# Kernel tuning notes

Measured on AMD Instinct MI355X. Metric: run time of the kernel, lower is better.

The kernel has to match this reference:

```python
import jax, jax.numpy as jnp
import numpy as np

B, S, D = 2, 2048, 1024
H = 16
HD = D // H


def setup_inputs() -> dict:
    key = jax.random.key(0)
    k1, k2, k3 = jax.random.split(key, 3)
    x = jax.random.normal(k1, (B, S, D), dtype=jnp.float32)
    # nn.Linear(d, 3d, bias=False): weight [3d, d]; y = x @ W.T
    w_qkv = jax.random.normal(k2, (3 * D, D), dtype=jnp.float32) * (D ** -0.5)
    w_out = jax.random.normal(k3, (D, D), dtype=jnp.float32) * (D ** -0.5)
    return {"x": x, "w_qkv": w_qkv, "w_out": w_out}


def reference(x, w_qkv, w_out):
    batch, seq_len, _ = x.shape
    qkv = jnp.einsum('bsd,ed->bse', x, w_qkv)  # [B,S,3D]
    q, k, v = jnp.split(qkv, 3, axis=-1)
    # [B,S,D] -> [B,H,S,HD]
    def heads(t):
        return t.reshape(batch, seq_len, H, HD).transpose(0, 2, 1, 3)
    q, k, v = heads(q), heads(k), heads(v)
    scale = HD ** -0.5
    attn = jnp.einsum('bhqd,bhkd->bhqk', q, k) * scale  # [B,H,S,S]
    causal = jnp.triu(jnp.ones((seq_len, seq_len), dtype=bool), k=1)
    attn = jnp.where(causal, -jnp.inf, attn)
    attn = jax.nn.softmax(attn, axis=-1)
    out = jnp.einsum('bhqk,bhkd->bhqd', attn, v)  # [B,H,S,HD]
    out = out.transpose(0, 2, 1, 3).reshape(batch, seq_len, D)
    return jnp.einsum('bsd,ed->bse', out, w_out)
```

## Files before the change

### kernel.cpp

```cpp
#include <hip/hip_runtime.h>

#define NUM_B 2
#define SEQ   2048
#define DIM   1024
#define NH    16
#define HD    64

typedef __attribute__((ext_vector_type(8))) short short8;
typedef __attribute__((ext_vector_type(4))) float floatx4;
typedef unsigned short us;

#define SOFTMAX_SHIFT 12.0f

__device__ __forceinline__ us f2bf(float f) {
    unsigned u = __float_as_uint(f);
    u += 0x7fffu + ((u >> 16) & 1u);
    return (us)(u >> 16);
}
__device__ __forceinline__ us f2bf_t(float f) {
    return (us)(__float_as_uint(f) >> 16);
}

#define GLD16(gptr, lptr) __builtin_amdgcn_global_load_lds( \
    (__attribute__((address_space(1))) unsigned int*)(gptr), \
    (__attribute__((address_space(3))) unsigned int*)(lptr), 16, 0, 0)

__global__ __launch_bounds__(256) void cast_all(
    const float* __restrict__ x, const float* __restrict__ wq,
    const float* __restrict__ wo, us* __restrict__ xb,
    us* __restrict__ wqb, us* __restrict__ wob)
{
    int i = blockIdx.x * 256 + threadIdx.x;
    const float* src; us* dst; int off;
    if (i < 524288)      { src = x;  dst = xb;  off = i; }
    else if (i < 917504) { src = wq; dst = wqb; off = i - 524288; }
    else                 { src = wo; dst = wob; off = i - 917504; }
    const float4* p = (const float4*)src + (size_t)off * 2;
    float4 f0 = p[0];
    float4 f1 = p[1];
    short8 v;
    v[0] = (short)f2bf(f0.x); v[1] = (short)f2bf(f0.y);
    v[2] = (short)f2bf(f0.z); v[3] = (short)f2bf(f0.w);
    v[4] = (short)f2bf(f1.x); v[5] = (short)f2bf(f1.y);
    v[6] = (short)f2bf(f1.z); v[7] = (short)f2bf(f1.w);
    *(short8*)(dst + (size_t)off * 8) = v;
}

__global__ __launch_bounds__(256, 2) void gemm_qkv(
    const us* __restrict__ A, const us* __restrict__ Bw,
    us* __restrict__ qb, us* __restrict__ kb, us* __restrict__ vt)
{
    __shared__ us As[128 * 64];
    __shared__ us Bs[128 * 64];
    const int t = threadIdx.x;
    const int lane = t & 63, w = t >> 6;
    const int l16 = lane & 15, quad = lane >> 4;
    const int wr = (w >> 1) * 64, wc = (w & 1) * 64;
    const int m0 = blockIdx.y * 128, n0 = blockIdx.x * 128;
    const bool isV = (blockIdx.x >= 16);
    const int srow = lane >> 3;
    const int soff = ((lane & 7) ^ srow) << 3;
    const int rsw  = l16 & 7;

    floatx4 acc[4][4];
    #pragma unroll
    for (int i = 0; i < 4; ++i)
        #pragma unroll
        for (int j = 0; j < 4; ++j) acc[i][j] = (floatx4){0.f, 0.f, 0.f, 0.f};

    for (int k0 = 0; k0 < DIM; k0 += 64) {
        #pragma unroll
        for (int c = 0; c < 4; ++c) {
            int chunk = w * 4 + c;
            int row = chunk * 8 + srow;
            GLD16(A  + (size_t)(m0 + row) * DIM + k0 + soff, &As[chunk * 512]);
            GLD16(Bw + (size_t)(n0 + row) * DIM + k0 + soff, &Bs[chunk * 512]);
        }
        __syncthreads();
        #pragma unroll
        for (int s = 0; s < 2; ++s) {
            short8 af[4], bf[4];
            #pragma unroll
            for (int i = 0; i < 4; ++i)
                af[i] = *(const short8*)&As[(wr + i * 16 + l16) * 64 + (((s * 4 + quad) ^ rsw) << 3)];
            #pragma unroll
            for (int j = 0; j < 4; ++j)
                bf[j] = *(const short8*)&Bs[(wc + j * 16 + l16) * 64 + (((s * 4 + quad) ^ rsw) << 3)];
            if (!isV) {
                #pragma unroll
                for (int i = 0; i < 4; ++i)
                    #pragma unroll
                    for (int j = 0; j < 4; ++j)
                        acc[i][j] = __builtin_amdgcn_mfma_f32_16x16x32_bf16(af[i], bf[j], acc[i][j], 0, 0, 0);
            } else {
                #pragma unroll
                for (int i = 0; i < 4; ++i)
                    #pragma unroll
                    for (int j = 0; j < 4; ++j)
                        acc[i][j] = __builtin_amdgcn_mfma_f32_16x16x32_bf16(bf[j], af[i], acc[i][j], 0, 0, 0);
            }
        }
        __syncthreads();
    }

    if (!isV) {
        const int which = n0 >> 10;
        const float sc = (which == 0) ? 0.125f : 1.0f;
        us* dst = (which == 0) ? qb : kb;
        #pragma unroll
        for (int i = 0; i < 4; ++i) {
            #pragma unroll
            for (int j = 0; j < 4; ++j) {
                int e = n0 + wc + j * 16 + l16;
                int h  = (e >> 6) & 15;
                int hd = e & 63;
                #pragma unroll
                for (int r = 0; r < 4; ++r) {
                    int m = m0 + wr + i * 16 + quad * 4 + r;
                    int b = m >> 11, s = m & 2047;
                    dst[((size_t)((b * NH + h) * SEQ + s) << 6) + hd] = f2bf(acc[i][j][r] * sc);
                }
            }
        }
    } else {
        #pragma unroll
        for (int i = 0; i < 4; ++i) {
            int m = m0 + wr + i * 16 + l16;
            int b = m >> 11, s = m & 2047;
            #pragma unroll
            for (int j = 0; j < 4; ++j) {
                int e0 = (n0 - 2048) + wc + j * 16 + quad * 4;
                #pragma unroll
                for (int r = 0; r < 4; ++r) {
                    int e = e0 + r;
                    int h = e >> 6, hd = e & 63;
                    vt[((size_t)((b * NH + h) * HD + hd) << 11) + s] = f2bf(acc[i][j][r]);
                }
            }
        }
    }
}

__global__ __launch_bounds__(256, 2) void gemm_out(
    const us* __restrict__ A, const us* __restrict__ Bw, float* __restrict__ outp)
{
    __shared__ us As[64 * 64];
    __shared__ us Bs[128 * 64];
    const int t = threadIdx.x;
    const int lane = t & 63, w = t >> 6;
    const int l16 = lane & 15, quad = lane >> 4;
    const int wr = (w >> 1) * 32, wc = (w & 1) * 64;
    const int m0 = blockIdx.y * 64, n0 = blockIdx.x * 128;
    const int srow = lane >> 3;
    const int soff = ((lane & 7) ^ srow) << 3;
    const int rsw  = l16 & 7;

    floatx4 acc[2][4];
    #pragma unroll
    for (int i = 0; i < 2; ++i)
        #pragma unroll
        for (int j = 0; j < 4; ++j) acc[i][j] = (floatx4){0.f, 0.f, 0.f, 0.f};

    for (int k0 = 0; k0 < DIM; k0 += 64) {
        #pragma unroll
        for (int c = 0; c < 2; ++c) {
            int chunk = w * 2 + c;
            int row = chunk * 8 + srow;
            GLD16(A + (size_t)(m0 + row) * DIM + k0 + soff, &As[chunk * 512]);
        }
        #pragma unroll
        for (int c = 0; c < 4; ++c) {
            int chunk = w * 4 + c;
            int row = chunk * 8 + srow;
            GLD16(Bw + (size_t)(n0 + row) * DIM + k0 + soff, &Bs[chunk * 512]);
        }
        __syncthreads();
        #pragma unroll
        for (int s = 0; s < 2; ++s) {
            short8 af[2], bf[4];
            #pragma unroll
            for (int i = 0; i < 2; ++i)
                af[i] = *(const short8*)&As[(wr + i * 16 + l16) * 64 + (((s * 4 + quad) ^ rsw) << 3)];
            #pragma unroll
            for (int j = 0; j < 4; ++j)
                bf[j] = *(const short8*)&Bs[(wc + j * 16 + l16) * 64 + (((s * 4 + quad) ^ rsw) << 3)];
            #pragma unroll
            for (int i = 0; i < 2; ++i)
                #pragma unroll
                for (int j = 0; j < 4; ++j)
                    acc[i][j] = __builtin_amdgcn_mfma_f32_16x16x32_bf16(af[i], bf[j], acc[i][j], 0, 0, 0);
        }
        __syncthreads();
    }

    #pragma unroll
    for (int i = 0; i < 2; ++i)
        #pragma unroll
        for (int j = 0; j < 4; ++j) {
            int n = n0 + wc + j * 16 + l16;
            #pragma unroll
            for (int r = 0; r < 4; ++r) {
                int m = m0 + wr + i * 16 + quad * 4 + r;
                outp[(size_t)m * DIM + n] = acc[i][j][r];
            }
        }
}

__global__ __launch_bounds__(256, 4) void attn(
    const us* __restrict__ qb, const us* __restrict__ kb,
    const us* __restrict__ vt, us* __restrict__ ob)
{
    __shared__ us Ks[2][64 * 64];
    __shared__ us Vs[2][64 * 64];
    __shared__ us Ps[4 * 16 * 72];
    const int t = threadIdx.x;
    const int lane = t & 63, w = t >> 6;
    const int l16 = lane & 15, quad = lane >> 4;
    const int idx = blockIdx.x;
    const int qt = 31 - (idx >> 5);
    const int bh = idx & 31;
    const int b = bh >> 4, h = bh & 15;
    const int q0 = qt << 6;
    const int r0 = q0 + w * 16;
    const int rowb = r0 + quad * 4;
    const size_t base = (size_t)bh * SEQ * HD;
    const us* qbh = qb + base;
    const us* kbh = kb + base;
    const us* vth = vt + base;
    us* Pp = Ps + w * 16 * 72;
    const int srow = lane >> 3;
    const int soff = ((lane & 7) ^ srow) << 3;
    const int rsw  = l16 & 7;

    short8 qa[2];
    #pragma unroll
    for (int s = 0; s < 2; ++s)
        qa[s] = *(const short8*)(qbh + (size_t)(r0 + l16) * HD + s * 32 + quad * 8);

    floatx4 o[4];
    #pragma unroll
    for (int j = 0; j < 4; ++j) o[j] = (floatx4){0.f, 0.f, 0.f, 0.f};
    float lrow[4] = {0.f, 0.f, 0.f, 0.f};

    #pragma unroll
    for (int c = 0; c < 2; ++c) {
        int chunk = w * 2 + c;
        int row = chunk * 8 + srow;
        GLD16(kbh + (size_t)row * HD + soff, &Ks[0][chunk * 512]);
        GLD16(vth + (size_t)row * SEQ + soff, &Vs[0][chunk * 512]);
    }
    __syncthreads();

    for (int kt = 0; kt <= qt; ++kt) {
        const int cur = kt & 1;
        if (kt < qt) {
            const int j0n = (kt + 1) << 6;
            #pragma unroll
            for (int c = 0; c < 2; ++c) {
                int chunk = w * 2 + c;
                int row = chunk * 8 + srow;
                GLD16(kbh + (size_t)(j0n + row) * HD + soff, &Ks[cur ^ 1][chunk * 512]);
                GLD16(vth + (size_t)row * SEQ + j0n + soff, &Vs[cur ^ 1][chunk * 512]);
            }
        }

        floatx4 sf[4];
        #pragma unroll
        for (int j = 0; j < 4; ++j)
            sf[j] = (floatx4){-SOFTMAX_SHIFT, -SOFTMAX_SHIFT, -SOFTMAX_SHIFT, -SOFTMAX_SHIFT};
        #pragma unroll
        for (int s = 0; s < 2; ++s)
            #pragma unroll
            for (int j = 0; j < 4; ++j) {
                short8 kf = *(const short8*)&Ks[cur][(j * 16 + l16) * 64 + (((s * 4 + quad) ^ rsw) << 3)];
                sf[j] = __builtin_amdgcn_mfma_f32_16x16x32_bf16(qa[s], kf, sf[j], 0, 0, 0);
            }

        float p[4][4];
        #pragma unroll
        for (int j = 0; j < 4; ++j)
            #pragma unroll
            for (int r = 0; r < 4; ++r) p[j][r] = sf[j][r];

        if (kt == qt) {
            const int j0 = kt << 6;
            #pragma unroll
            for (int j = 0; j < 4; ++j) {
                int colg = j0 + j * 16 + l16;
                #pragma unroll
                for (int r = 0; r < 4; ++r)
                    if (colg > rowb + r) p[j][r] = -1e30f;
            }
        }

        #pragma unroll
        for (int j = 0; j < 4; ++j)
            #pragma unroll
            for (int r = 0; r < 4; ++r) {
                p[j][r] = __expf(p[j][r]);
                Pp[(quad * 4 + r) * 72 + j * 16 + l16] = f2bf_t(p[j][r]);
            }
        #pragma unroll
        for (int r = 0; r < 4; ++r)
            lrow[r] += (p[0][r] + p[1][r]) + (p[2][r] + p[3][r]);

        #pragma unroll
        for (int s = 0; s < 2; ++s) {
            short8 pf = *(const short8*)&Pp[l16 * 72 + s * 32 + quad * 8];
            #pragma unroll
            for (int j = 0; j < 4; ++j) {
                short8 vf = *(const short8*)&Vs[cur][(j * 16 + l16) * 64 + (((s * 4 + quad) ^ rsw) << 3)];
                o[j] = __builtin_amdgcn_mfma_f32_16x16x32_bf16(pf, vf, o[j], 0, 0, 0);
            }
        }
        __syncthreads();
    }

    #pragma unroll
    for (int r = 0; r < 4; ++r) {
        float l = lrow[r];
        l += __shfl_xor(l, 1);
        l += __shfl_xor(l, 2);
        l += __shfl_xor(l, 4);
        l += __shfl_xor(l, 8);
        float inv = 1.0f / l;
        #pragma unroll
        for (int j = 0; j < 4; ++j) {
            float val = o[j][r] * inv;
            ob[(size_t)(b * SEQ + rowb + r) * DIM + h * HD + j * 16 + l16] = f2bf(val);
        }
    }
}

extern "C" void kernel_launch(void* const* d_in, const int* in_sizes, int n_in,
                              void* d_out, int out_size, void* d_ws, size_t ws_size,
                              hipStream_t stream) {
    const float* x     = (const float*)d_in[0];
    const float* w_qkv = (const float*)d_in[1];
    const float* w_out = (const float*)d_in[2];
    float* out = (float*)d_out;
    us* ws = (us*)d_ws;

    const size_t M1 = (size_t)1024 * 1024;
    us* xb  = ws;
    us* wqb = xb  + 4 * M1;
    us* wob = wqb + 3 * M1;
    us* qb  = wob + 1 * M1;
    us* kb  = qb  + 4 * M1;
    us* vt  = kb  + 4 * M1;
    us* obf = vt  + 4 * M1;

    cast_all<<<4096, 256, 0, stream>>>(x, w_qkv, w_out, xb, wqb, wob);
    gemm_qkv<<<dim3(24, 32), 256, 0, stream>>>(xb, wqb, qb, kb, vt);
    attn<<<1024, 256, 0, stream>>>(qb, kb, vt, obf);
    gemm_out<<<dim3(8, 64), 256, 0, stream>>>(obf, wob, out);
}
```

Baseline: 170.0 us.

## Rewrite QKV GEMM as 256x256 double-buffered 8-wave pipeline; add MFMA priority hints

The QKV projection GEMM moves from 128x128 tiles with 4 waves and a single LDS buffer to 256x256 tiles with 8 waves and double-buffered LDS. Each K-step is split into four quadrant phases, with global-to-LDS loads of the next tile interleaved and fenced by explicit vmcnt waits and barriers. s_setprio is raised around MFMA blocks in both the GEMM and the attention kernel. The goal is to hide load latency and raise per-block operand reuse, at the cost of only 192 blocks on the GPU, 128 KB of LDS per block, and heavy accumulator register pressure.

After: 189.7 us. 1.12x slower.

```diff
diff --git a/kernel.cpp b/kernel.cpp
--- a/kernel.cpp
+++ b/kernel.cpp
@@ -24,6 +24,10 @@
 #define GLD16(gptr, lptr) __builtin_amdgcn_global_load_lds( \
     (__attribute__((address_space(1))) unsigned int*)(gptr), \
     (__attribute__((address_space(3))) unsigned int*)(lptr), 16, 0, 0)
+
+#define VMW(n) asm volatile("s_waitcnt vmcnt(" #n ")" ::: "memory")
+#define BAR()  __builtin_amdgcn_s_barrier()
+#define SETP(p) __builtin_amdgcn_s_setprio(p)
 
 __global__ __launch_bounds__(256) void cast_all(
     const float* __restrict__ x, const float* __restrict__ wq,
@@ -46,61 +50,104 @@
     *(short8*)(dst + (size_t)off * 8) = v;
 }
 
-__global__ __launch_bounds__(256, 2) void gemm_qkv(
+__global__ __launch_bounds__(512, 2) void gemm_qkv(
     const us* __restrict__ A, const us* __restrict__ Bw,
     us* __restrict__ qb, us* __restrict__ kb, us* __restrict__ vt)
 {
-    __shared__ us As[128 * 64];
-    __shared__ us Bs[128 * 64];
+    __shared__ us As[2][256 * 64];
+    __shared__ us Bs[2][256 * 64];
     const int t = threadIdx.x;
     const int lane = t & 63, w = t >> 6;
     const int l16 = lane & 15, quad = lane >> 4;
-    const int wr = (w >> 1) * 64, wc = (w & 1) * 64;
-    const int m0 = blockIdx.y * 128, n0 = blockIdx.x * 128;
-    const bool isV = (blockIdx.x >= 16);
+    const int wr = (w >> 2) * 128, wc = (w & 3) * 64;
+    const int m0 = blockIdx.y * 256, n0 = blockIdx.x * 256;
+    const bool isV = (n0 >= 2048);
     const int srow = lane >> 3;
     const int soff = ((lane & 7) ^ srow) << 3;
     const int rsw  = l16 & 7;
-
-    floatx4 acc[4][4];
-    #pragma unroll
-    for (int i = 0; i < 4; ++i)
+    const int rbA = (w >> 2) * 128 + (w & 3) * 16;
+    const int cbA = (w >> 2) * 16 + (w & 3) * 2;
+    const int rbB = (w & 3) * 64 + (w >> 2) * 16;
+    const int cbB = (w & 3) * 8 + (w >> 2) * 2;
+
+#define SA(bufi, kti, h) do { _Pragma("unroll") \
+    for (int c = 0; c < 2; ++c) \
+        GLD16(A + (size_t)(m0 + rbA + (h) * 64 + c * 8 + srow) * DIM + (kti) * 64 + soff, \
+              &As[bufi][(cbA + (h) * 8 + c) * 512]); } while (0)
+#define SB(bufi, kti, h) do { _Pragma("unroll") \
+    for (int c = 0; c < 2; ++c) \
+        GLD16(Bw + (size_t)(n0 + rbB + (h) * 32 + c * 8 + srow) * DIM + (kti) * 64 + soff, \
+              &Bs[bufi][(cbB + (h) * 4 + c) * 512]); } while (0)
+#define RDA(bufi, i, s) (*(const short8*)&As[bufi][(wr + (i) * 16 + l16) * 64 + ((((s) * 4 + quad) ^ rsw) << 3)])
+#define RDB(bufi, j, s) (*(const short8*)&Bs[bufi][(wc + (j) * 16 + l16) * 64 + ((((s) * 4 + quad) ^ rsw) << 3)])
+#define MMCL(AF, BF, I0, J0) do { \
+    if (!isV) { \
+        _Pragma("unroll") for (int s = 0; s < 2; ++s) \
+        _Pragma("unroll") for (int i = 0; i < 4; ++i) \
+        _Pragma("unroll") for (int j = 0; j < 2; ++j) \
+            acc[(I0) + i][(J0) + j] = __builtin_amdgcn_mfma_f32_16x16x32_bf16( \
+                AF[i][s], BF[j][s], acc[(I0) + i][(J0) + j], 0, 0, 0); \
+    } else { \
+        _Pragma("unroll") for (int s = 0; s < 2; ++s) \
+        _Pragma("unroll") for (int i = 0; i < 4; ++i) \
+        _Pragma("unroll") for (int j = 0; j < 2; ++j) \
+            acc[(I0) + i][(J0) + j] = __builtin_amdgcn_mfma_f32_16x16x32_bf16( \
+                BF[j][s], AF[i][s], acc[(I0) + i][(J0) + j], 0, 0, 0); \
+    } } while (0)
+
+    floatx4 acc[8][4];
+    #pragma unroll
+    for (int i = 0; i < 8; ++i)
         #pragma unroll
         for (int j = 0; j < 4; ++j) acc[i][j] = (floatx4){0.f, 0.f, 0.f, 0.f};
 
-    for (int k0 = 0; k0 < DIM; k0 += 64) {
-        #pragma unroll
-        for (int c = 0; c < 4; ++c) {
-            int chunk = w * 4 + c;
-            int row = chunk * 8 + srow;
-            GLD16(A  + (size_t)(m0 + row) * DIM + k0 + soff, &As[chunk * 512]);
-            GLD16(Bw + (size_t)(n0 + row) * DIM + k0 + soff, &Bs[chunk * 512]);
-        }
-        __syncthreads();
-        #pragma unroll
-        for (int s = 0; s < 2; ++s) {
-            short8 af[4], bf[4];
-            #pragma unroll
-            for (int i = 0; i < 4; ++i)
-                af[i] = *(const short8*)&As[(wr + i * 16 + l16) * 64 + (((s * 4 + quad) ^ rsw) << 3)];
-            #pragma unroll
-            for (int j = 0; j < 4; ++j)
-                bf[j] = *(const short8*)&Bs[(wc + j * 16 + l16) * 64 + (((s * 4 + quad) ^ rsw) << 3)];
-            if (!isV) {
-                #pragma unroll
-                for (int i = 0; i < 4; ++i)
-                    #pragma unroll
-                    for (int j = 0; j < 4; ++j)
-                        acc[i][j] = __builtin_amdgcn_mfma_f32_16x16x32_bf16(af[i], bf[j], acc[i][j], 0, 0, 0);
-            } else {
-                #pragma unroll
-                for (int i = 0; i < 4; ++i)
-                    #pragma unroll
-                    for (int j = 0; j < 4; ++j)
-                        acc[i][j] = __builtin_amdgcn_mfma_f32_16x16x32_bf16(bf[j], af[i], acc[i][j], 0, 0, 0);
-            }
-        }
-        __syncthreads();
+    SA(0, 0, 0);
+    SB(0, 0, 0);
+    SB(0, 0, 1);
+    SA(0, 0, 1);
+    VMW(4);
+    BAR();
+
+    for (int kt = 0; kt < 16; ++kt) {
+        const int cur = kt & 1, nxt = cur ^ 1;
+        const int ktn = (kt + 1) & 15;
+
+        short8 a0[4][2], b0[2][2];
+        #pragma unroll
+        for (int i = 0; i < 4; ++i) { a0[i][0] = RDA(cur, i, 0); a0[i][1] = RDA(cur, i, 1); }
+        #pragma unroll
+        for (int j = 0; j < 2; ++j) { b0[j][0] = RDB(cur, j, 0); b0[j][1] = RDB(cur, j, 1); }
+        SA(nxt, ktn, 0);
+        VMW(4);
+        BAR();
+        SETP(1); MMCL(a0, b0, 0, 0); SETP(0);
+        BAR();
+
+        short8 b1[2][2];
+        #pragma unroll
+        for (int j = 0; j < 2; ++j) { b1[j][0] = RDB(cur, j + 2, 0); b1[j][1] = RDB(cur, j + 2, 1); }
+        SB(nxt, ktn, 0);
+        VMW(4);
+        BAR();
+        SETP(1); MMCL(a0, b1, 0, 2); SETP(0);
+        BAR();
+
+        short8 a1[4][2];
+        #pragma unroll
+        for (int i = 0; i < 4; ++i) { a1[i][0] = RDA(cur, i + 4, 0); a1[i][1] = RDA(cur, i + 4, 1); }
+        SB(nxt, ktn, 1);
+        BAR();
+        SETP(1); MMCL(a1, b1, 4, 2); SETP(0);
+        BAR();
+
+        short8 b0b[2][2];
+        #pragma unroll
+        for (int j = 0; j < 2; ++j) { b0b[j][0] = RDB(cur, j, 0); b0b[j][1] = RDB(cur, j, 1); }
+        SA(nxt, ktn, 1);
+        VMW(4);
+        BAR();
+        SETP(1); MMCL(a1, b0b, 4, 0); SETP(0);
+        BAR();
     }
 
     if (!isV) {
@@ -108,7 +155,7 @@
         const float sc = (which == 0) ? 0.125f : 1.0f;
         us* dst = (which == 0) ? qb : kb;
         #pragma unroll
-        for (int i = 0; i < 4; ++i) {
+        for (int i = 0; i < 8; ++i) {
             #pragma unroll
             for (int j = 0; j < 4; ++j) {
                 int e = n0 + wc + j * 16 + l16;
@@ -124,7 +171,7 @@
         }
     } else {
         #pragma unroll
-        for (int i = 0; i < 4; ++i) {
+        for (int i = 0; i < 8; ++i) {
             int m = m0 + wr + i * 16 + l16;
             int b = m >> 11, s = m & 2047;
             #pragma unroll
@@ -139,6 +186,11 @@
             }
         }
     }
+#undef SA
+#undef SB
+#undef RDA
+#undef RDB
+#undef MMCL
 }
 
 __global__ __launch_bounds__(256, 2) void gemm_out(
@@ -268,6 +320,7 @@
         #pragma unroll
         for (int j = 0; j < 4; ++j)
             sf[j] = (floatx4){-SOFTMAX_SHIFT, -SOFTMAX_SHIFT, -SOFTMAX_SHIFT, -SOFTMAX_SHIFT};
+        SETP(1);
         #pragma unroll
         for (int s = 0; s < 2; ++s)
             #pragma unroll
@@ -275,6 +328,7 @@
                 short8 kf = *(const short8*)&Ks[cur][(j * 16 + l16) * 64 + (((s * 4 + quad) ^ rsw) << 3)];
                 sf[j] = __builtin_amdgcn_mfma_f32_16x16x32_bf16(qa[s], kf, sf[j], 0, 0, 0);
             }
+        SETP(0);
 
         float p[4][4];
         #pragma unroll
@@ -304,6 +358,7 @@
         for (int r = 0; r < 4; ++r)
             lrow[r] += (p[0][r] + p[1][r]) + (p[2][r] + p[3][r]);
 
+        SETP(1);
         #pragma unroll
         for (int s = 0; s < 2; ++s) {
             short8 pf = *(const short8*)&Pp[l16 * 72 + s * 32 + quad * 8];
@@ -313,6 +368,7 @@
                 o[j] = __builtin_amdgcn_mfma_f32_16x16x32_bf16(pf, vf, o[j], 0, 0, 0);
             }
         }
+        SETP(0);
         __syncthreads();
     }
 
@@ -351,7 +407,7 @@
     us* obf = vt  + 4 * M1;
 
     cast_all<<<4096, 256, 0, stream>>>(x, w_qkv, w_out, xb, wqb, wob);
-    gemm_qkv<<<dim3(24, 32), 256, 0, stream>>>(xb, wqb, qb, kb, vt);
+    gemm_qkv<<<dim3(12, 16), 512, 0, stream>>>(xb, wqb, qb, kb, vt);
     attn<<<1024, 256, 0, stream>>>(qb, kb, vt, obf);
     gemm_out<<<dim3(8, 64), 256, 0, stream>>>(obf, wob, out);
 }
```
